# Optimization experiments

Measured on AMD Instinct MI355X. Metric: run time of the kernel, lower is better.

Reference implementation:

```python
import math
import jax, jax.numpy as jnp
import numpy as np

B, T, C, H, E, K = 2, 2048, 1024, 16, 8, 2
HID = 4 * C
D = C // H

def new_gelu(x):
    return 0.5 * x * (1.0 + jnp.tanh(math.sqrt(2.0 / math.pi) * (x + 0.044715 * x ** 3)))

def layer_norm(x, g, b, eps=1e-5):
    mu = jnp.mean(x, axis=-1, keepdims=True)
    var = jnp.var(x, axis=-1, keepdims=True)
    return (x - mu) / jnp.sqrt(var + eps) * g + b

def setup_inputs():
    key = jax.random.key(0)
    ks = jax.random.split(key, 8)
    s = 0.02
    return {
        'x': jax.random.normal(ks[0], (B, T, C), jnp.float32),
        'ln1_g': jnp.ones((C,), jnp.float32), 'ln1_b': jnp.zeros((C,), jnp.float32),
        'ln2_g': jnp.ones((C,), jnp.float32), 'ln2_b': jnp.zeros((C,), jnp.float32),
        'attn_w': (jax.random.normal(ks[1], (C, 3 * C), jnp.float32) * s),
        'attn_b': jnp.zeros((3 * C,), jnp.float32),
        'proj_w': (jax.random.normal(ks[2], (C, C), jnp.float32) * s),
        'proj_b': jnp.zeros((C,), jnp.float32),
        'router_w': (jax.random.normal(ks[3], (C, E), jnp.float32) * s),
        'fc_w': (jax.random.normal(ks[4], (E, C, HID), jnp.float32) * s),
        'fc_b': jnp.zeros((E, HID), jnp.float32),
        'pj_w': (jax.random.normal(ks[5], (E, HID, C), jnp.float32) * s),
        'pj_b': jnp.zeros((E, C), jnp.float32),
    }

def reference(x, ln1_g, ln1_b, ln2_g, ln2_b, attn_w, attn_b, proj_w, proj_b, router_w, fc_w, fc_b, pj_w, pj_b):
    # --- causal self-attention with residual ---
    h = layer_norm(x, ln1_g, ln1_b)
    qkv = h @ attn_w + attn_b                              # [B,T,3C]
    q, k, v = jnp.split(qkv, 3, axis=-1)
    q = q.reshape(B, T, H, D).transpose(0, 2, 1, 3)        # [B,H,T,D]
    k = k.reshape(B, T, H, D).transpose(0, 2, 1, 3)
    v = v.reshape(B, T, H, D).transpose(0, 2, 1, 3)
    att = jnp.einsum('bhqd,bhkd->bhqk', q, k) * (1.0 / math.sqrt(D))
    mask = jnp.tril(jnp.ones((T, T), dtype=bool))
    att = jnp.where(mask, att, jnp.float32(-jnp.inf))
    att = jax.nn.softmax(att, axis=-1)                     # dropout p=0 (eval)
    y = jnp.einsum('bhqk,bhkd->bhqd', att, v)
    y = y.transpose(0, 2, 1, 3).reshape(B, T, C)
    x = x + (y @ proj_w + proj_b)
    # --- MoE FFN with residual ---
    h2 = layer_norm(x, ln2_g, ln2_b).reshape(B * T, C)     # [N,C]
    logits = h2 @ router_w                                 # [N,E]
    probs = jax.nn.softmax(logits, axis=-1)
    topk_p, topk_i = jax.lax.top_k(probs, K)               # [N,K]
    topk_p = topk_p / jnp.sum(topk_p, axis=-1, keepdims=True)
    # dense combine weights: zero outside selected experts (same math as scatter)
    gate = jnp.zeros((B * T, E), h2.dtype).at[jnp.arange(B * T)[:, None], topk_i].add(topk_p)
    out = jnp.zeros_like(h2)
    for e in range(E):  # fixed small expert loop
        he = new_gelu(h2 @ fc_w[e] + fc_b[e])              # [N,HID]
        out = out + gate[:, e:e + 1] * (he @ pj_w[e] + pj_b[e])
    return x + out.reshape(B, T, C)
```

## Files before the change

### kernel.cpp

```cpp
#include <hip/hip_runtime.h>
#include <math.h>


typedef __bf16 b16v8 __attribute__((ext_vector_type(8)));
typedef float f32x4 __attribute__((ext_vector_type(4)));

#define MFMA(a, b, c) __builtin_amdgcn_mfma_f32_16x16x32_bf16(a, b, c, 0, 0, 0)

#define GLOAD_LDS16(g, l)                                          \
  __builtin_amdgcn_global_load_lds(                                \
      (const __attribute__((address_space(1))) void*)(g),          \
      (__attribute__((address_space(3))) void*)(l), 16, 0, 0)

#define SYNC_VM0()                                       \
  do {                                                   \
    asm volatile("s_waitcnt vmcnt(0)" ::: "memory");     \
    __builtin_amdgcn_s_barrier();                        \
    asm volatile("" ::: "memory");                       \
  } while (0)

constexpr int Bc = 2, Tc = 2048, Cc = 1024, Hc = 16, Dc = 64;
constexpr int Nc = Bc * Tc;
constexpr int HIDc = 4096;
constexpr int Ec = 8;
constexpr int NPAIR = Nc * 2;
constexpr float LOG2E = 1.4426950408889634f;

__device__ inline unsigned short f32_bf16(float f) {
  union { float f; unsigned u; } x; x.f = f;
  unsigned r = x.u + 0x7fffu + ((x.u >> 16) & 1u);
  return (unsigned short)(r >> 16);
}

__device__ inline float gelu_f(float x) {
  float t = 2.3021188f * x * (1.f + 0.044715f * x * x);
  float e = __builtin_amdgcn_exp2f(-t);
  return x * __builtin_amdgcn_rcpf(1.f + e);
}

__global__ __launch_bounds__(256) void convT_kernel(
    const float* __restrict__ src, unsigned short* __restrict__ dst,
    int K, int N) {
  const size_t sb = (size_t)blockIdx.z * K * N;
  const int n0 = blockIdx.x * 32, k0 = blockIdx.y * 32;
  __shared__ float t[32][33];
  const int tx = threadIdx.x & 31, ty = threadIdx.x >> 5;
#pragma unroll
  for (int j = 0; j < 4; ++j)
    t[ty + j * 8][tx] = src[sb + (size_t)(k0 + ty + j * 8) * N + n0 + tx];
  __syncthreads();
#pragma unroll
  for (int j = 0; j < 4; ++j)
    dst[sb + (size_t)(n0 + ty + j * 8) * K + k0 + tx] = f32_bf16(t[tx][ty + j * 8]);
}

__global__ __launch_bounds__(256) void ln1_kernel(
    const float* __restrict__ x, const float* __restrict__ g,
    const float* __restrict__ b, unsigned short* __restrict__ out) {
  const int row = blockIdx.x;
  const int tid = threadIdx.x;
  const float* xr = x + (size_t)row * Cc;
  float v[4]; float s = 0.f, q = 0.f;
#pragma unroll
  for (int j = 0; j < 4; ++j) { v[j] = xr[tid + j * 256]; s += v[j]; q += v[j] * v[j]; }
#pragma unroll
  for (int m = 1; m <= 32; m <<= 1) { s += __shfl_xor(s, m); q += __shfl_xor(q, m); }
  __shared__ float red[2][4];
  const int w = tid >> 6;
  if ((tid & 63) == 0) { red[0][w] = s; red[1][w] = q; }
  __syncthreads();
  s = red[0][0] + red[0][1] + red[0][2] + red[0][3];
  q = red[1][0] + red[1][1] + red[1][2] + red[1][3];
  const float mean = s * (1.f / Cc);
  const float var = q * (1.f / Cc) - mean * mean;
  const float rstd = rsqrtf(var + 1e-5f);
#pragma unroll
  for (int j = 0; j < 4; ++j) {
    int c = tid + j * 256;
    out[(size_t)row * Cc + c] = f32_bf16((v[j] - mean) * rstd * g[c] + b[c]);
  }
}

__global__ __launch_bounds__(256) void ln2_router_kernel(
    const float* __restrict__ x, const float* __restrict__ g,
    const float* __restrict__ b, const float* __restrict__ rw,
    unsigned short* __restrict__ out, int* __restrict__ tki, float* __restrict__ tkp) {
  const int row = blockIdx.x;
  const int tid = threadIdx.x;
  const float* xr = x + (size_t)row * Cc;
  float v[4]; float s = 0.f, q = 0.f;
#pragma unroll
  for (int j = 0; j < 4; ++j) { v[j] = xr[tid + j * 256]; s += v[j]; q += v[j] * v[j]; }
#pragma unroll
  for (int m = 1; m <= 32; m <<= 1) { s += __shfl_xor(s, m); q += __shfl_xor(q, m); }
  __shared__ float red[2][4];
  const int w = tid >> 6;
  if ((tid & 63) == 0) { red[0][w] = s; red[1][w] = q; }
  __syncthreads();
  s = red[0][0] + red[0][1] + red[0][2] + red[0][3];
  q = red[1][0] + red[1][1] + red[1][2] + red[1][3];
  const float mean = s * (1.f / Cc);
  const float var = q * (1.f / Cc) - mean * mean;
  const float rstd = rsqrtf(var + 1e-5f);
  float lg[8] = {0.f, 0.f, 0.f, 0.f, 0.f, 0.f, 0.f, 0.f};
#pragma unroll
  for (int j = 0; j < 4; ++j) {
    int c = tid + j * 256;
    float nv = (v[j] - mean) * rstd * g[c] + b[c];
    out[(size_t)row * Cc + c] = f32_bf16(nv);
    const float* rwc = rw + c * 8;
#pragma unroll
    for (int e = 0; e < 8; ++e) lg[e] += nv * rwc[e];
  }
#pragma unroll
  for (int m = 1; m <= 32; m <<= 1) {
#pragma unroll
    for (int e = 0; e < 8; ++e) lg[e] += __shfl_xor(lg[e], m);
  }
  __shared__ float rl[4][8];
  if ((tid & 63) == 0) {
#pragma unroll
    for (int e = 0; e < 8; ++e) rl[w][e] = lg[e];
  }
  __syncthreads();
  if (tid == 0) {
    float L[8];
#pragma unroll
    for (int e = 0; e < 8; ++e) L[e] = rl[0][e] + rl[1][e] + rl[2][e] + rl[3][e];
    int i1 = 0;
    for (int e = 1; e < 8; ++e) if (L[e] > L[i1]) i1 = e;
    int i2 = (i1 == 0) ? 1 : 0;
    for (int e = 0; e < 8; ++e) if (e != i1 && L[e] > L[i2]) i2 = e;
    float e2 = expf(L[i2] - L[i1]);
    float inv = 1.f / (1.f + e2);
    tki[row * 2] = i1; tki[row * 2 + 1] = i2;
    tkp[row * 2] = inv; tkp[row * 2 + 1] = e2 * inv;
  }
}

__global__ __launch_bounds__(256) void count_kernel(
    const int* __restrict__ tki, int* __restrict__ counts) {
  int n = blockIdx.x * 256 + threadIdx.x;
  if (n >= Nc) return;
  atomicAdd(&counts[tki[n * 2]], 1);
  atomicAdd(&counts[tki[n * 2 + 1]], 1);
}

__global__ void scan_kernel(const int* __restrict__ counts,
                            int* __restrict__ eoff, int* __restrict__ cursor) {
  if (threadIdx.x == 0 && blockIdx.x == 0) {
    int s = 0;
    for (int e = 0; e < Ec; ++e) { eoff[e] = s; cursor[e] = s; s += counts[e]; }
    eoff[Ec] = s;
  }
}

__global__ __launch_bounds__(256) void assign_kernel(
    const int* __restrict__ tki, int* __restrict__ cursor,
    int* __restrict__ slot_tok, int* __restrict__ tok2slot) {
  int n = blockIdx.x * 256 + threadIdx.x;
  if (n >= Nc) return;
#pragma unroll
  for (int kk = 0; kk < 2; ++kk) {
    int e = tki[n * 2 + kk];
    int slot = atomicAdd(&cursor[e], 1);
    slot_tok[slot] = n;
    tok2slot[n * 2 + kk] = slot;
  }
}

struct GArgs {
  const unsigned short* A;
  const unsigned short* Bt;
  const float* bias;
  int M, N, K, lda;
  size_t Bstride; int biasStride;
  const int* eoff;
  const int* slot_tok;
  float* outF;
  const float* resid;
  unsigned short* outB;
  unsigned short* outK;
  unsigned short* outV;
};

template <int MODE>
__global__ __launch_bounds__(256) void gemm128(GArgs g) {
  const int e = blockIdx.z;
  int s0 = 0, Meff = g.M;
  if constexpr (MODE == 2 || MODE == 3) {
    s0 = g.eoff[e];
    Meff = g.eoff[e + 1] - s0;
  }
  const int row0 = blockIdx.y * 128;
  if (row0 >= Meff) return;
  const int col0 = blockIdx.x * 128;

  __shared__ __align__(16) unsigned short As[2][4096];
  __shared__ __align__(16) unsigned short Bs[2][4096];

  const int tid = threadIdx.x;
  const int lane = tid & 63, w = tid >> 6;
  const int wr = w >> 1, wc = w & 1;
  const int fr = lane & 15, fg = lane >> 4;

  const unsigned short* Bt = g.Bt + (size_t)e * g.Bstride;
  const float* bias = g.bias + (size_t)e * g.biasStride;

  size_t aaddr[2], baddr[2];
#pragma unroll
  for (int i = 0; i < 2; ++i) {
    int pos = i * 256 + tid;
    int r = pos >> 2, c8 = (pos & 3) * 8;
    int gr = row0 + r;
    if (gr >= Meff) gr = Meff - 1;
    int srcrow;
    if constexpr (MODE == 2) srcrow = g.slot_tok[s0 + gr];
    else if constexpr (MODE == 3) srcrow = s0 + gr;
    else srcrow = gr;
    aaddr[i] = (size_t)srcrow * g.lda + c8;
    baddr[i] = (size_t)(col0 + r) * g.K + c8;
  }

  auto STAGE = [&](int buf, int k0) {
#pragma unroll
    for (int i = 0; i < 2; ++i) {
      GLOAD_LDS16(g.A + aaddr[i] + k0, &As[buf][i * 2048 + w * 512]);
      GLOAD_LDS16(Bt + baddr[i] + k0, &Bs[buf][i * 2048 + w * 512]);
    }
  };

  f32x4 acc[4][4] = {};
  const int nt = g.K / 32;

  STAGE(0, 0);
  SYNC_VM0();
  int cur = 0;

  for (int t = 0; t < nt; ++t) {
    if (t + 1 < nt) STAGE(cur ^ 1, (t + 1) * 32);
    b16v8 af[4], bfr[4];
#pragma unroll
    for (int mi = 0; mi < 4; ++mi)
      af[mi] = *(const b16v8*)&As[cur][(wr * 64 + mi * 16 + fr) * 32 + fg * 8];
#pragma unroll
    for (int ni = 0; ni < 4; ++ni)
      bfr[ni] = *(const b16v8*)&Bs[cur][(wc * 64 + ni * 16 + fr) * 32 + fg * 8];
#pragma unroll
    for (int mi = 0; mi < 4; ++mi)
#pragma unroll
      for (int ni = 0; ni < 4; ++ni)
        acc[mi][ni] = MFMA(af[mi], bfr[ni], acc[mi][ni]);
    if (t + 1 < nt) {
      SYNC_VM0();
      cur ^= 1;
    }
  }

#pragma unroll
  for (int mi = 0; mi < 4; ++mi) {
#pragma unroll
    for (int ni = 0; ni < 4; ++ni) {
#pragma unroll
      for (int rr = 0; rr < 4; ++rr) {
        int row = row0 + wr * 64 + mi * 16 + fg * 4 + rr;
        int col = col0 + wc * 64 + ni * 16 + fr;
        if (row >= Meff) continue;
        float val = acc[mi][ni][rr] + bias[col];
        if constexpr (MODE == 0) {
          int bb = row >> 11, t = row & (Tc - 1);
          int which = col >> 10, cj = col & (Cc - 1);
          int hd = cj >> 6, d = cj & 63;
          if (which == 0)
            g.outB[(((size_t)(bb * Hc + hd)) * Tc + t) * Dc + d] = f32_bf16(val);
          else if (which == 1)
            g.outK[(((size_t)(bb * Hc + hd)) * Tc + t) * Dc + d] = f32_bf16(val);
          else
            g.outV[(((size_t)(bb * Hc + hd)) * Dc + d) * Tc + t] = f32_bf16(val);
        } else if constexpr (MODE == 1) {
          size_t o = (size_t)row * g.N + col;
          g.outF[o] = val + g.resid[o];
        } else if constexpr (MODE == 2) {
          g.outB[(size_t)(s0 + row) * g.N + col] = f32_bf16(gelu_f(val));
        } else {
          g.outF[(size_t)(s0 + row) * g.N + col] = val;
        }
      }
    }
  }
}

__global__ __launch_bounds__(256) void attn_kernel(
    const unsigned short* __restrict__ q, const unsigned short* __restrict__ k,
    const unsigned short* __restrict__ v, unsigned short* __restrict__ y) {
  const int qt = blockIdx.x, bh = blockIdx.y;
  const int qbase = qt * 64;
  __shared__ __align__(16) unsigned short ldsK[64][72];
  __shared__ __align__(16) unsigned short ldsVT[64][72];
  __shared__ __align__(16) unsigned short ldsP[4][16][72];
  const int tid = threadIdx.x, lane = tid & 63, w = tid >> 6;
  const int fr = lane & 15, fg = lane >> 4;
  const size_t base = (size_t)bh * Tc * Dc;
  const int qrow = qbase + w * 16 + fr;
  b16v8 qa0 = *(const b16v8*)(q + base + (size_t)qrow * Dc + fg * 8);
  b16v8 qa1 = *(const b16v8*)(q + base + (size_t)qrow * Dc + 32 + fg * 8);
  float m[4], lsum[4] = {0.f, 0.f, 0.f, 0.f};
#pragma unroll
  for (int r = 0; r < 4; ++r) m[r] = -3.0e38f;
  f32x4 oacc[4] = {};
  constexpr float SC = 0.125f * LOG2E;

  for (int kb = 0; kb <= qbase; kb += 64) {
    __syncthreads();
#pragma unroll
    for (int i = 0; i < 2; ++i) {
      int pos = i * 256 + tid;
      int r = pos >> 3, cb = (pos & 7) * 8;
      *(uint4*)&ldsK[r][cb]  = *(const uint4*)(k + base + (size_t)(kb + r) * Dc + cb);
      *(uint4*)&ldsVT[r][cb] = *(const uint4*)(v + base + (size_t)r * Tc + kb + cb);
    }
    __syncthreads();

    f32x4 s[4];
#pragma unroll
    for (int ni = 0; ni < 4; ++ni) {
      b16v8 kb0 = *(const b16v8*)&ldsK[ni * 16 + fr][fg * 8];
      b16v8 kb1 = *(const b16v8*)&ldsK[ni * 16 + fr][32 + fg * 8];
      f32x4 z = {};
      z = MFMA(qa0, kb0, z);
      z = MFMA(qa1, kb1, z);
      s[ni] = z;
    }
    const bool diag = (kb == qbase);
#pragma unroll
    for (int ni = 0; ni < 4; ++ni) {
#pragma unroll
      for (int r = 0; r < 4; ++r) {
        float sv = s[ni][r] * SC;
        if (diag) {
          int qr = w * 16 + fg * 4 + r;
          int kc = ni * 16 + fr;
          if (kc > qr) sv = -3.0e38f;
        }
        s[ni][r] = sv;
      }
    }
#pragma unroll
    for (int r = 0; r < 4; ++r) {
      float mx = fmaxf(fmaxf(s[0][r], s[1][r]), fmaxf(s[2][r], s[3][r]));
#pragma unroll
      for (int msk = 1; msk <= 8; msk <<= 1) mx = fmaxf(mx, __shfl_xor(mx, msk));
      float mnew = fmaxf(m[r], mx);
      float alpha = __builtin_amdgcn_exp2f(m[r] - mnew);
      float psum = 0.f;
#pragma unroll
      for (int ni = 0; ni < 4; ++ni) {
        float pp = __builtin_amdgcn_exp2f(s[ni][r] - mnew);
        s[ni][r] = pp;
        psum += pp;
      }
#pragma unroll
      for (int msk = 1; msk <= 8; msk <<= 1) psum += __shfl_xor(psum, msk);
      lsum[r] = lsum[r] * alpha + psum;
      m[r] = mnew;
#pragma unroll
      for (int ni = 0; ni < 4; ++ni) {
        oacc[ni][r] = oacc[ni][r] * alpha;
        ldsP[w][fg * 4 + r][ni * 16 + fr] = f32_bf16(s[ni][r]);
      }
    }
    asm volatile("s_waitcnt lgkmcnt(0)" ::: "memory");
    __builtin_amdgcn_sched_barrier(0);
    b16v8 pa0 = *(const b16v8*)&ldsP[w][fr][fg * 8];
    b16v8 pa1 = *(const b16v8*)&ldsP[w][fr][32 + fg * 8];
#pragma unroll
    for (int ni = 0; ni < 4; ++ni) {
      b16v8 vb0 = *(const b16v8*)&ldsVT[ni * 16 + fr][fg * 8];
      b16v8 vb1 = *(const b16v8*)&ldsVT[ni * 16 + fr][32 + fg * 8];
      oacc[ni] = MFMA(pa0, vb0, oacc[ni]);
      oacc[ni] = MFMA(pa1, vb1, oacc[ni]);
    }
  }

  const int bb = bh >> 4, hh = bh & 15;
#pragma unroll
  for (int r = 0; r < 4; ++r) {
    float rl = __builtin_amdgcn_rcpf(lsum[r]);
#pragma unroll
    for (int ni = 0; ni < 4; ++ni) {
      int t = qbase + w * 16 + fg * 4 + r;
      int d = ni * 16 + fr;
      y[((size_t)(bb * Tc + t)) * Cc + hh * Dc + d] = f32_bf16(oacc[ni][r] * rl);
    }
  }
}

__global__ __launch_bounds__(256) void combine_kernel(
    const float* __restrict__ pair, const float* __restrict__ tkp,
    const int* __restrict__ tok2slot, float* __restrict__ out) {
  const int n = blockIdx.x;
  const int c4 = threadIdx.x * 4;
  const int s0 = tok2slot[n * 2], s1 = tok2slot[n * 2 + 1];
  const float p0 = tkp[n * 2], p1 = tkp[n * 2 + 1];
  float4 a = *(const float4*)&pair[(size_t)s0 * Cc + c4];
  float4 b = *(const float4*)&pair[(size_t)s1 * Cc + c4];
  float4 o = *(float4*)&out[(size_t)n * Cc + c4];
  o.x += p0 * a.x + p1 * b.x;
  o.y += p0 * a.y + p1 * b.y;
  o.z += p0 * a.z + p1 * b.z;
  o.w += p0 * a.w + p1 * b.w;
  *(float4*)&out[(size_t)n * Cc + c4] = o;
}

extern "C" void kernel_launch(void* const* d_in, const int* in_sizes, int n_in,
                              void* d_out, int out_size, void* d_ws, size_t ws_size,
                              hipStream_t stream) {
  const float* x        = (const float*)d_in[0];
  const float* ln1_g    = (const float*)d_in[1];
  const float* ln1_b    = (const float*)d_in[2];
  const float* ln2_g    = (const float*)d_in[3];
  const float* ln2_b    = (const float*)d_in[4];
  const float* attn_w   = (const float*)d_in[5];
  const float* attn_b   = (const float*)d_in[6];
  const float* proj_w   = (const float*)d_in[7];
  const float* proj_b   = (const float*)d_in[8];
  const float* router_w = (const float*)d_in[9];
  const float* fc_w     = (const float*)d_in[10];
  const float* fc_b     = (const float*)d_in[11];
  const float* pj_w     = (const float*)d_in[12];
  const float* pj_b     = (const float*)d_in[13];
  float* out = (float*)d_out;

  char* ws = (char*)d_ws;
  size_t off = 0;
  auto alloc = [&](size_t bytes) -> void* {
    void* p = ws + off;
    off = (off + bytes + 255) & ~(size_t)255;
    return p;
  };
  unsigned short* attn_wT = (unsigned short*)alloc((size_t)3 * Cc * Cc * 2);
  unsigned short* proj_wT = (unsigned short*)alloc((size_t)Cc * Cc * 2);
  unsigned short* fc_wT   = (unsigned short*)alloc((size_t)Ec * HIDc * Cc * 2);
  unsigned short* pj_wT   = (unsigned short*)alloc((size_t)Ec * Cc * HIDc * 2);
  unsigned short* h    = (unsigned short*)alloc((size_t)Nc * Cc * 2);
  unsigned short* qb   = (unsigned short*)alloc((size_t)Nc * Cc * 2);
  unsigned short* kbuf = (unsigned short*)alloc((size_t)Nc * Cc * 2);
  unsigned short* vbuf = (unsigned short*)alloc((size_t)Nc * Cc * 2);
  unsigned short* ybuf = (unsigned short*)alloc((size_t)Nc * Cc * 2);
  unsigned short* he   = (unsigned short*)alloc((size_t)NPAIR * HIDc * 2);
  float* pairout = (float*)alloc((size_t)NPAIR * Cc * 4);
  int*   tki     = (int*)alloc((size_t)Nc * 2 * 4);
  float* tkp     = (float*)alloc((size_t)Nc * 2 * 4);
  int*   counts  = (int*)alloc(Ec * 4);
  int*   eoff    = (int*)alloc((Ec + 1) * 4);
  int*   cursor  = (int*)alloc(Ec * 4);
  int*   slot_tok= (int*)alloc((size_t)NPAIR * 4);
  int*   tok2slot= (int*)alloc((size_t)Nc * 2 * 4);
  (void)ws_size; (void)in_sizes; (void)n_in; (void)out_size;

  convT_kernel<<<dim3(3 * Cc / 32, Cc / 32, 1), 256, 0, stream>>>(attn_w, attn_wT, Cc, 3 * Cc);
  convT_kernel<<<dim3(Cc / 32, Cc / 32, 1), 256, 0, stream>>>(proj_w, proj_wT, Cc, Cc);
  convT_kernel<<<dim3(HIDc / 32, Cc / 32, Ec), 256, 0, stream>>>(fc_w, fc_wT, Cc, HIDc);
  convT_kernel<<<dim3(Cc / 32, HIDc / 32, Ec), 256, 0, stream>>>(pj_w, pj_wT, HIDc, Cc);

  ln1_kernel<<<Nc, 256, 0, stream>>>(x, ln1_g, ln1_b, h);

  {
    GArgs a = {};
    a.A = h; a.Bt = attn_wT; a.bias = attn_b;
    a.M = Nc; a.N = 3 * Cc; a.K = Cc; a.lda = Cc;
    a.outB = qb; a.outK = kbuf; a.outV = vbuf;
    gemm128<0><<<dim3(3 * Cc / 128, Nc / 128, 1), 256, 0, stream>>>(a);
  }

  attn_kernel<<<dim3(Tc / 64, Bc * Hc), 256, 0, stream>>>(qb, kbuf, vbuf, ybuf);

  {
    GArgs p = {};
    p.A = ybuf; p.Bt = proj_wT; p.bias = proj_b;
    p.M = Nc; p.N = Cc; p.K = Cc; p.lda = Cc;
    p.outF = out; p.resid = x;
    gemm128<1><<<dim3(Cc / 128, Nc / 128, 1), 256, 0, stream>>>(p);
  }

  ln2_router_kernel<<<Nc, 256, 0, stream>>>(out, ln2_g, ln2_b, router_w, h, tki, tkp);

  hipMemsetAsync(counts, 0, Ec * sizeof(int), stream);
  count_kernel<<<(Nc + 255) / 256, 256, 0, stream>>>(tki, counts);
  scan_kernel<<<1, 64, 0, stream>>>(counts, eoff, cursor);
  assign_kernel<<<(Nc + 255) / 256, 256, 0, stream>>>(tki, cursor, slot_tok, tok2slot);

  {
    GArgs f = {};
    f.A = h; f.Bt = fc_wT; f.bias = fc_b;
    f.M = Nc; f.N = HIDc; f.K = Cc; f.lda = Cc;
    f.Bstride = (size_t)HIDc * Cc; f.biasStride = HIDc;
    f.eoff = eoff; f.slot_tok = slot_tok;
    f.outB = he;
    gemm128<2><<<dim3(HIDc / 128, Nc / 128, Ec), 256, 0, stream>>>(f);
  }

  {
    GArgs pj = {};
    pj.A = he; pj.Bt = pj_wT; pj.bias = pj_b;
    pj.M = Nc; pj.N = Cc; pj.K = HIDc; pj.lda = HIDc;
    pj.Bstride = (size_t)Cc * HIDc; pj.biasStride = Cc;
    pj.eoff = eoff;
    pj.outF = pairout;
    gemm128<3><<<dim3(Cc / 128, Nc / 128, Ec), 256, 0, stream>>>(pj);
  }

  combine_kernel<<<Nc, 256, 0, stream>>>(pairout, tkp, tok2slot, out);
}
```

Before: 681.7 us.

## Use 256x256 GEMM tiles, split-K expert projection, and 128-row attention blocks

The QKV, expert FC and expert projection GEMMs move to a 512-thread kernel with 256x256 tiles and a 64-deep K step, which raises data reuse per LDS load. The expert projection is split along K into two halves that write separate partial buffers, and the combine kernel sums them, so more blocks exist for that small-M grouped GEMM. Attention blocks now cover 128 query rows with 8 waves, and each wave applies its own causal mask. The output projection keeps a dedicated 128-tile kernel. The larger tiles use more LDS and registers, which risks occupancy and leaves partially filled tiles for experts with few tokens, and split-K adds extra fp32 traffic.

```diff
diff --git a/kernel.cpp b/kernel.cpp
--- a/kernel.cpp
+++ b/kernel.cpp
@@ -173,7 +173,7 @@
   const unsigned short* A;
   const unsigned short* Bt;
   const float* bias;
-  int M, N, K, lda;
+  int M, N, K, lda, ldb, klen;
   size_t Bstride; int biasStride;
   const int* eoff;
   const int* slot_tok;
@@ -185,48 +185,146 @@
 };
 
 template <int MODE>
-__global__ __launch_bounds__(256) void gemm128(GArgs g) {
-  const int e = blockIdx.z;
+__global__ __launch_bounds__(512) void gemm256(GArgs g) {
+  const int zz = blockIdx.z;
+  const int e  = (MODE == 3) ? (zz & 7) : zz;
+  const int kh = (MODE == 3) ? (zz >> 3) : 0;
   int s0 = 0, Meff = g.M;
   if constexpr (MODE == 2 || MODE == 3) {
     s0 = g.eoff[e];
     Meff = g.eoff[e + 1] - s0;
   }
-  const int row0 = blockIdx.y * 128;
+  const int row0 = blockIdx.y * 256;
   if (row0 >= Meff) return;
-  const int col0 = blockIdx.x * 128;
-
-  __shared__ __align__(16) unsigned short As[2][4096];
-  __shared__ __align__(16) unsigned short Bs[2][4096];
+  const int col0 = blockIdx.x * 256;
+  const int kbase = kh * g.klen;
+
+  __shared__ __align__(16) unsigned short As[2][256 * 64];
+  __shared__ __align__(16) unsigned short Bs[2][256 * 64];
 
   const int tid = threadIdx.x;
   const int lane = tid & 63, w = tid >> 6;
-  const int wr = w >> 1, wc = w & 1;
+  const int wr = w >> 2, wc = w & 3;
   const int fr = lane & 15, fg = lane >> 4;
 
   const unsigned short* Bt = g.Bt + (size_t)e * g.Bstride;
   const float* bias = g.bias + (size_t)e * g.biasStride;
 
-  size_t aaddr[2], baddr[2];
-#pragma unroll
-  for (int i = 0; i < 2; ++i) {
-    int pos = i * 256 + tid;
-    int r = pos >> 2, c8 = (pos & 3) * 8;
+  size_t aaddr[4], baddr[4];
+#pragma unroll
+  for (int i = 0; i < 4; ++i) {
+    int pos = i * 512 + tid;
+    int r = pos >> 3, c8 = (pos & 7) * 8;
     int gr = row0 + r;
     if (gr >= Meff) gr = Meff - 1;
     int srcrow;
     if constexpr (MODE == 2) srcrow = g.slot_tok[s0 + gr];
     else if constexpr (MODE == 3) srcrow = s0 + gr;
     else srcrow = gr;
-    aaddr[i] = (size_t)srcrow * g.lda + c8;
-    baddr[i] = (size_t)(col0 + r) * g.K + c8;
+    aaddr[i] = (size_t)srcrow * g.lda + kbase + c8;
+    baddr[i] = (size_t)(col0 + r) * g.ldb + kbase + c8;
+  }
+
+  auto STAGE = [&](int buf, int k0) {
+#pragma unroll
+    for (int i = 0; i < 4; ++i) {
+      GLOAD_LDS16(g.A + aaddr[i] + k0, &As[buf][i * 4096 + w * 512]);
+      GLOAD_LDS16(Bt + baddr[i] + k0, &Bs[buf][i * 4096 + w * 512]);
+    }
+  };
+
+  f32x4 acc[8][4] = {};
+  const int nt = g.klen / 64;
+
+  STAGE(0, 0);
+  SYNC_VM0();
+  int cur = 0;
+
+  for (int t = 0; t < nt; ++t) {
+    if (t + 1 < nt) STAGE(cur ^ 1, (t + 1) * 64);
+    b16v8 bfrag[4][2];
+#pragma unroll
+    for (int ni = 0; ni < 4; ++ni)
+#pragma unroll
+      for (int ks = 0; ks < 2; ++ks)
+        bfrag[ni][ks] = *(const b16v8*)&Bs[cur][(wc * 64 + ni * 16 + fr) * 64 + ks * 32 + fg * 8];
+#pragma unroll
+    for (int mi = 0; mi < 8; ++mi) {
+      b16v8 a0 = *(const b16v8*)&As[cur][(wr * 128 + mi * 16 + fr) * 64 + fg * 8];
+      b16v8 a1 = *(const b16v8*)&As[cur][(wr * 128 + mi * 16 + fr) * 64 + 32 + fg * 8];
+#pragma unroll
+      for (int ni = 0; ni < 4; ++ni) {
+        acc[mi][ni] = MFMA(a0, bfrag[ni][0], acc[mi][ni]);
+        acc[mi][ni] = MFMA(a1, bfrag[ni][1], acc[mi][ni]);
+      }
+    }
+    if (t + 1 < nt) {
+      SYNC_VM0();
+      cur ^= 1;
+    }
+  }
+
+  float* outF3 = nullptr;
+  if constexpr (MODE == 3) outF3 = g.outF + (size_t)kh * NPAIR * Cc;
+
+#pragma unroll
+  for (int mi = 0; mi < 8; ++mi) {
+#pragma unroll
+    for (int ni = 0; ni < 4; ++ni) {
+#pragma unroll
+      for (int rr = 0; rr < 4; ++rr) {
+        int row = row0 + wr * 128 + mi * 16 + fg * 4 + rr;
+        int col = col0 + wc * 64 + ni * 16 + fr;
+        if (row >= Meff) continue;
+        float bval = bias[col];
+        if constexpr (MODE == 3) { if (kh != 0) bval = 0.f; }
+        float val = acc[mi][ni][rr] + bval;
+        if constexpr (MODE == 0) {
+          int bb = row >> 11, tt = row & (Tc - 1);
+          int which = col >> 10, cj = col & (Cc - 1);
+          int hd = cj >> 6, d = cj & 63;
+          if (which == 0)
+            g.outB[(((size_t)(bb * Hc + hd)) * Tc + tt) * Dc + d] = f32_bf16(val);
+          else if (which == 1)
+            g.outK[(((size_t)(bb * Hc + hd)) * Tc + tt) * Dc + d] = f32_bf16(val);
+          else
+            g.outV[(((size_t)(bb * Hc + hd)) * Dc + d) * Tc + tt] = f32_bf16(val);
+        } else if constexpr (MODE == 2) {
+          g.outB[(size_t)(s0 + row) * g.N + col] = f32_bf16(gelu_f(val));
+        } else {
+          outF3[(size_t)(s0 + row) * g.N + col] = val;
+        }
+      }
+    }
+  }
+}
+
+__global__ __launch_bounds__(256) void gemm128_proj(GArgs g) {
+  const int row0 = blockIdx.y * 128;
+  const int col0 = blockIdx.x * 128;
+
+  __shared__ __align__(16) unsigned short As[2][4096];
+  __shared__ __align__(16) unsigned short Bs[2][4096];
+
+  const int tid = threadIdx.x;
+  const int lane = tid & 63, w = tid >> 6;
+  const int wr = w >> 1, wc = w & 1;
+  const int fr = lane & 15, fg = lane >> 4;
+
+  size_t aaddr[2], baddr[2];
+#pragma unroll
+  for (int i = 0; i < 2; ++i) {
+    int pos = i * 256 + tid;
+    int r = pos >> 2, c8 = (pos & 3) * 8;
+    aaddr[i] = (size_t)(row0 + r) * g.lda + c8;
+    baddr[i] = (size_t)(col0 + r) * g.ldb + c8;
   }
 
   auto STAGE = [&](int buf, int k0) {
 #pragma unroll
     for (int i = 0; i < 2; ++i) {
       GLOAD_LDS16(g.A + aaddr[i] + k0, &As[buf][i * 2048 + w * 512]);
-      GLOAD_LDS16(Bt + baddr[i] + k0, &Bs[buf][i * 2048 + w * 512]);
+      GLOAD_LDS16(g.Bt + baddr[i] + k0, &Bs[buf][i * 2048 + w * 512]);
     }
   };
 
@@ -265,39 +363,21 @@
       for (int rr = 0; rr < 4; ++rr) {
         int row = row0 + wr * 64 + mi * 16 + fg * 4 + rr;
         int col = col0 + wc * 64 + ni * 16 + fr;
-        if (row >= Meff) continue;
-        float val = acc[mi][ni][rr] + bias[col];
-        if constexpr (MODE == 0) {
-          int bb = row >> 11, t = row & (Tc - 1);
-          int which = col >> 10, cj = col & (Cc - 1);
-          int hd = cj >> 6, d = cj & 63;
-          if (which == 0)
-            g.outB[(((size_t)(bb * Hc + hd)) * Tc + t) * Dc + d] = f32_bf16(val);
-          else if (which == 1)
-            g.outK[(((size_t)(bb * Hc + hd)) * Tc + t) * Dc + d] = f32_bf16(val);
-          else
-            g.outV[(((size_t)(bb * Hc + hd)) * Dc + d) * Tc + t] = f32_bf16(val);
-        } else if constexpr (MODE == 1) {
-          size_t o = (size_t)row * g.N + col;
-          g.outF[o] = val + g.resid[o];
-        } else if constexpr (MODE == 2) {
-          g.outB[(size_t)(s0 + row) * g.N + col] = f32_bf16(gelu_f(val));
-        } else {
-          g.outF[(size_t)(s0 + row) * g.N + col] = val;
-        }
+        size_t o = (size_t)row * g.N + col;
+        g.outF[o] = acc[mi][ni][rr] + g.bias[col] + g.resid[o];
       }
     }
   }
 }
 
-__global__ __launch_bounds__(256) void attn_kernel(
+__global__ __launch_bounds__(512) void attn_kernel(
     const unsigned short* __restrict__ q, const unsigned short* __restrict__ k,
     const unsigned short* __restrict__ v, unsigned short* __restrict__ y) {
   const int qt = blockIdx.x, bh = blockIdx.y;
-  const int qbase = qt * 64;
+  const int qbase = qt * 128;
   __shared__ __align__(16) unsigned short ldsK[64][72];
   __shared__ __align__(16) unsigned short ldsVT[64][72];
-  __shared__ __align__(16) unsigned short ldsP[4][16][72];
+  __shared__ __align__(16) unsigned short ldsP[8][16][72];
   const int tid = threadIdx.x, lane = tid & 63, w = tid >> 6;
   const int fr = lane & 15, fg = lane >> 4;
   const size_t base = (size_t)bh * Tc * Dc;
@@ -310,15 +390,12 @@
   f32x4 oacc[4] = {};
   constexpr float SC = 0.125f * LOG2E;
 
-  for (int kb = 0; kb <= qbase; kb += 64) {
+  const int sr = tid >> 3, scb = (tid & 7) * 8;
+
+  for (int kb = 0; kb < qbase + 128; kb += 64) {
     __syncthreads();
-#pragma unroll
-    for (int i = 0; i < 2; ++i) {
-      int pos = i * 256 + tid;
-      int r = pos >> 3, cb = (pos & 7) * 8;
-      *(uint4*)&ldsK[r][cb]  = *(const uint4*)(k + base + (size_t)(kb + r) * Dc + cb);
-      *(uint4*)&ldsVT[r][cb] = *(const uint4*)(v + base + (size_t)r * Tc + kb + cb);
-    }
+    *(uint4*)&ldsK[sr][scb]  = *(const uint4*)(k + base + (size_t)(kb + sr) * Dc + scb);
+    *(uint4*)&ldsVT[sr][scb] = *(const uint4*)(v + base + (size_t)sr * Tc + kb + scb);
     __syncthreads();
 
     f32x4 s[4];
@@ -331,16 +408,16 @@
       z = MFMA(qa1, kb1, z);
       s[ni] = z;
     }
-    const bool diag = (kb == qbase);
+    const bool diag = (kb + 64 > qbase + w * 16);
 #pragma unroll
     for (int ni = 0; ni < 4; ++ni) {
 #pragma unroll
       for (int r = 0; r < 4; ++r) {
         float sv = s[ni][r] * SC;
         if (diag) {
-          int qr = w * 16 + fg * 4 + r;
-          int kc = ni * 16 + fr;
-          if (kc > qr) sv = -3.0e38f;
+          int gq = qbase + w * 16 + fg * 4 + r;
+          int kv = kb + ni * 16 + fr;
+          if (kv > gq) sv = -3.0e38f;
         }
         s[ni][r] = sv;
       }
@@ -402,13 +479,16 @@
   const int c4 = threadIdx.x * 4;
   const int s0 = tok2slot[n * 2], s1 = tok2slot[n * 2 + 1];
   const float p0 = tkp[n * 2], p1 = tkp[n * 2 + 1];
-  float4 a = *(const float4*)&pair[(size_t)s0 * Cc + c4];
-  float4 b = *(const float4*)&pair[(size_t)s1 * Cc + c4];
+  const float* pb = pair + (size_t)NPAIR * Cc;
+  float4 a0 = *(const float4*)&pair[(size_t)s0 * Cc + c4];
+  float4 a1 = *(const float4*)&pb[(size_t)s0 * Cc + c4];
+  float4 b0 = *(const float4*)&pair[(size_t)s1 * Cc + c4];
+  float4 b1 = *(const float4*)&pb[(size_t)s1 * Cc + c4];
   float4 o = *(float4*)&out[(size_t)n * Cc + c4];
-  o.x += p0 * a.x + p1 * b.x;
-  o.y += p0 * a.y + p1 * b.y;
-  o.z += p0 * a.z + p1 * b.z;
-  o.w += p0 * a.w + p1 * b.w;
+  o.x += p0 * (a0.x + a1.x) + p1 * (b0.x + b1.x);
+  o.y += p0 * (a0.y + a1.y) + p1 * (b0.y + b1.y);
+  o.z += p0 * (a0.z + a1.z) + p1 * (b0.z + b1.z);
+  o.w += p0 * (a0.w + a1.w) + p1 * (b0.w + b1.w);
   *(float4*)&out[(size_t)n * Cc + c4] = o;
 }
 
@@ -448,7 +528,7 @@
   unsigned short* vbuf = (unsigned short*)alloc((size_t)Nc * Cc * 2);
   unsigned short* ybuf = (unsigned short*)alloc((size_t)Nc * Cc * 2);
   unsigned short* he   = (unsigned short*)alloc((size_t)NPAIR * HIDc * 2);
-  float* pairout = (float*)alloc((size_t)NPAIR * Cc * 4);
+  float* pairout = (float*)alloc((size_t)2 * NPAIR * Cc * 4);
   int*   tki     = (int*)alloc((size_t)Nc * 2 * 4);
   float* tkp     = (float*)alloc((size_t)Nc * 2 * 4);
   int*   counts  = (int*)alloc(Ec * 4);
@@ -468,19 +548,19 @@
   {
     GArgs a = {};
     a.A = h; a.Bt = attn_wT; a.bias = attn_b;
-    a.M = Nc; a.N = 3 * Cc; a.K = Cc; a.lda = Cc;
+    a.M = Nc; a.N = 3 * Cc; a.K = Cc; a.lda = Cc; a.ldb = Cc; a.klen = Cc;
     a.outB = qb; a.outK = kbuf; a.outV = vbuf;
-    gemm128<0><<<dim3(3 * Cc / 128, Nc / 128, 1), 256, 0, stream>>>(a);
-  }
-
-  attn_kernel<<<dim3(Tc / 64, Bc * Hc), 256, 0, stream>>>(qb, kbuf, vbuf, ybuf);
+    gemm256<0><<<dim3(3 * Cc / 256, Nc / 256, 1), 512, 0, stream>>>(a);
+  }
+
+  attn_kernel<<<dim3(Tc / 128, Bc * Hc), 512, 0, stream>>>(qb, kbuf, vbuf, ybuf);
 
   {
     GArgs p = {};
     p.A = ybuf; p.Bt = proj_wT; p.bias = proj_b;
-    p.M = Nc; p.N = Cc; p.K = Cc; p.lda = Cc;
+    p.M = Nc; p.N = Cc; p.K = Cc; p.lda = Cc; p.ldb = Cc; p.klen = Cc;
     p.outF = out; p.resid = x;
-    gemm128<1><<<dim3(Cc / 128, Nc / 128, 1), 256, 0, stream>>>(p);
+    gemm128_proj<<<dim3(Cc / 128, Nc / 128, 1), 256, 0, stream>>>(p);
   }
 
   ln2_router_kernel<<<Nc, 256, 0, stream>>>(out, ln2_g, ln2_b, router_w, h, tki, tkp);
@@ -493,21 +573,21 @@
   {
     GArgs f = {};
     f.A = h; f.Bt = fc_wT; f.bias = fc_b;
-    f.M = Nc; f.N = HIDc; f.K = Cc; f.lda = Cc;
+    f.M = Nc; f.N = HIDc; f.K = Cc; f.lda = Cc; f.ldb = Cc; f.klen = Cc;
     f.Bstride = (size_t)HIDc * Cc; f.biasStride = HIDc;
     f.eoff = eoff; f.slot_tok = slot_tok;
     f.outB = he;
-    gemm128<2><<<dim3(HIDc / 128, Nc / 128, Ec), 256, 0, stream>>>(f);
+    gemm256<2><<<dim3(HIDc / 256, Nc / 256, Ec), 512, 0, stream>>>(f);
   }
 
   {
     GArgs pj = {};
     pj.A = he; pj.Bt = pj_wT; pj.bias = pj_b;
-    pj.M = Nc; pj.N = Cc; pj.K = HIDc; pj.lda = HIDc;
+    pj.M = Nc; pj.N = Cc; pj.K = HIDc; pj.lda = HIDc; pj.ldb = HIDc; pj.klen = HIDc / 2;
     pj.Bstride = (size_t)Cc * HIDc; pj.biasStride = Cc;
     pj.eoff = eoff;
     pj.outF = pairout;
-    gemm128<3><<<dim3(Cc / 128, Nc / 128, Ec), 256, 0, stream>>>(pj);
+    gemm256<3><<<dim3(Cc / 256, Nc / 256, 2 * Ec), 512, 0, stream>>>(pj);
   }
 
   combine_kernel<<<Nc, 256, 0, stream>>>(pairout, tkp, tok2slot, out);
```

Result: slower. 794.3 us (+16.5%).
